# Kernel tuning notes

Measured on AMD Instinct MI355X. Metric: run time of the kernel, lower is better.

Reference implementation:

```python
import jax, jax.numpy as jnp
import numpy as np

N, E, R, H = 50000, 800000, 8, 1  # nodes, edges, relations, heads
IN_DIM = HID = OUT = 128
NEG_SLOPE = 0.2  # PyG RGATConv default


def _rgat_layer(x, W, q, k, b, src, dst, etype):
    """One RGATConv (additive-self-attention, across-relation softmax, dim=1).
    x: [N, Cin]; W: [R, Cin, H*C]; q,k: [H*C, H]; b: [H*C]."""
    n = x.shape[0]
    xr = jnp.einsum('nc,rcd->rnd', x, W)            # [R, N, H*C] per-relation transform
    qproj = jnp.einsum('rnd,dh->rnh', xr, q)        # [R, N, H]
    kproj = jnp.einsum('rnd,dh->rnh', xr, k)        # [R, N, H]
    out_j = xr[etype, src]                          # [E, H*C] transformed source feats
    alpha = jax.nn.leaky_relu(qproj[etype, dst] + kproj[etype, src], NEG_SLOPE)  # [E, H]
    # per-destination-node softmax over incoming edges (across relations)
    amax = jax.ops.segment_max(alpha, dst, num_segments=n)
    amax = jnp.where(jnp.isfinite(amax), amax, 0.0)
    ex = jnp.exp(alpha - amax[dst])                 # [E, H]
    denom = jax.ops.segment_sum(ex, dst, num_segments=n)
    alpha = ex / (denom[dst] + 1e-16)
    d = out_j.shape[1]
    c = d // H
    msg = (alpha[:, :, None] * out_j.reshape(-1, H, c)).reshape(-1, d)  # [E, H*C]
    out = jax.ops.segment_sum(msg, dst, num_segments=n)                  # [N, H*C]
    return out + b


def setup_inputs() -> dict:
    key = jax.random.key(0)
    ks = jax.random.split(key, 16)
    inp = {
        'x': jax.random.normal(ks[0], (N, IN_DIM), dtype=jnp.float32),
        'edge_index': jax.random.randint(ks[1], (2, E), 0, N, dtype=jnp.int32),
        'edge_type': jax.random.randint(ks[2], (E,), 0, R, dtype=jnp.int32),
    }
    dims = [(IN_DIM, HID), (HID, HID), (HID, OUT)]
    for i, (cin, cout) in enumerate(dims):
        d = H * cout
        s = 1.0 / np.sqrt(cin)
        inp[f'W{i}'] = jax.random.normal(ks[3 + 4 * i], (R, cin, d), dtype=jnp.float32) * s
        inp[f'q{i}'] = jax.random.normal(ks[4 + 4 * i], (d, H), dtype=jnp.float32) * (1.0 / np.sqrt(d))
        inp[f'k{i}'] = jax.random.normal(ks[5 + 4 * i], (d, H), dtype=jnp.float32) * (1.0 / np.sqrt(d))
        inp[f'b{i}'] = jnp.zeros((d,), dtype=jnp.float32)
    return inp


def reference(x, edge_index, edge_type, W0, q0, k0, b0, W1, q1, k1, b1, W2, q2, k2, b2):
    src, dst = edge_index[0], edge_index[1]
    h = jax.nn.relu(_rgat_layer(x, W0, q0, k0, b0, src, dst, edge_type))
    h = jax.nn.relu(_rgat_layer(h, W1, q1, k1, b1, src, dst, edge_type))
    return _rgat_layer(h, W2, q2, k2, b2, src, dst, edge_type)
```

## Files before the change

kernel.cpp:

```cpp
#include <hip/hip_runtime.h>
#include <hip/hip_bf16.h>
#include <cstdint>
#include <cstddef>

#define NNODES 50000
#define NEDGES 800000
#define NREL 8
#define DIM 128
#define NOUT 1024
#define NEG_SLOPE 0.2f

typedef __attribute__((ext_vector_type(8))) short short8;
typedef __attribute__((ext_vector_type(4))) float f32x4;

static __device__ __forceinline__ short f2bf(float v) {
  union { float f; unsigned u; } c; c.f = v;
  unsigned u = c.u;
  unsigned r = (u + 0x7fffu + ((u >> 16) & 1u)) >> 16;
  return (short)r;
}
static __device__ __forceinline__ float bf2f(short s) {
  union { unsigned u; float f; } c; c.u = ((unsigned)(unsigned short)s) << 16;
  return c.f;
}


__global__ void k_hist(const int* __restrict__ ei, const int* __restrict__ et,
                       int* __restrict__ cnt, int E) {
  int e = blockIdx.x * 256 + threadIdx.x;
  if (e < E) {
    int d = ei[E + e];
    int t = et[e];
    atomicAdd(&cnt[d * NREL + t], 1);
  }
}

__global__ void k_scan_reduce(const int* __restrict__ cnt, int* __restrict__ sums, int n) {
  __shared__ int sd[256];
  int base = blockIdx.x * 4096;
  int t = threadIdx.x;
  int acc = 0;
  for (int i = t; i < 4096; i += 256) {
    int idx = base + i;
    if (idx < n) acc += cnt[idx];
  }
  sd[t] = acc; __syncthreads();
  for (int s = 128; s > 0; s >>= 1) {
    if (t < s) sd[t] += sd[t + s];
    __syncthreads();
  }
  if (t == 0) sums[blockIdx.x] = sd[0];
}

__global__ void k_scan_top(int* sums, int nb) {
  if (threadIdx.x == 0 && blockIdx.x == 0) {
    int run = 0;
    for (int i = 0; i < nb; i++) { int v = sums[i]; sums[i] = run; run += v; }
  }
}

__global__ void k_scan_final(const int* __restrict__ cnt, const int* __restrict__ sums,
                             int* __restrict__ offs, int n, int E) {
  __shared__ int sd[256];
  int base = blockIdx.x * 4096;
  int t = threadIdx.x;
  int run = sums[blockIdx.x];
  for (int c = 0; c < 16; c++) {
    int idx = base + c * 256 + t;
    int v = (idx < n) ? cnt[idx] : 0;
    sd[t] = v; __syncthreads();
    for (int s = 1; s < 256; s <<= 1) {
      int u = (t >= s) ? sd[t - s] : 0;
      __syncthreads();
      sd[t] += u;
      __syncthreads();
    }
    if (idx < n) offs[idx] = run + sd[t] - v;
    run += sd[255];
    __syncthreads();
  }
  if (blockIdx.x == 0 && t == 0) offs[n] = E;
}

__global__ void k_scatter(const int* __restrict__ ei, const int* __restrict__ et,
                          int* __restrict__ cursor, int* __restrict__ pk, int E) {
  int e = blockIdx.x * 256 + threadIdx.x;
  if (e < E) {
    int s = ei[e];
    int d = ei[E + e];
    int t = et[e];
    int pos = atomicAdd(&cursor[d * NREL + t], 1);
    pk[pos] = s | (t << 16);
  }
}


__global__ void k_splitW_frag(const float* __restrict__ W, short* __restrict__ Wfh,
                              short* __restrict__ Wfl) {
  int id = blockIdx.x * 256 + threadIdx.x;
  if (id >= 16384) return;
  int l = id & 63;
  int kc = (id >> 6) & 3;
  int n16 = id >> 8;
  int n = n16 * 16 + (l & 15);
  int r = n >> 7, nn = n & 127;
  int k0 = kc * 32 + (l >> 4) * 8;
  short8 vh, vl;
#pragma unroll
  for (int j = 0; j < 8; j++) {
    float v = W[((size_t)r * DIM + k0 + j) * DIM + nn];
    short h = f2bf(v);
    vh[j] = h;
    vl[j] = f2bf(v - bf2f(h));
  }
  ((short8*)Wfh)[id] = vh;
  ((short8*)Wfl)[id] = vl;
}

__global__ void k_wqk(const float* __restrict__ W, const float* __restrict__ q,
                      const float* __restrict__ k, float* __restrict__ wq,
                      float* __restrict__ wk) {
  int id = blockIdx.x * 256 + threadIdx.x;
  if (id >= 2 * NREL * DIM) return;
  int which = id >> 10;
  int rc = id & 1023;
  const float* wrow = W + (size_t)rc * DIM;
  const float* v = which ? k : q;
  float acc = 0.f;
#pragma unroll 8
  for (int d = 0; d < DIM; d++) acc += wrow[d] * v[d];
  (which ? wk : wq)[rc] = acc;
}

__global__ void k_qk(const float* __restrict__ x, const float* __restrict__ wq,
                     const float* __restrict__ wk, float* __restrict__ qp,
                     float* __restrict__ kp, int N) {
  int wid = (blockIdx.x * blockDim.x + threadIdx.x) >> 6;
  int lane = threadIdx.x & 63;
  if (wid >= N) return;
  float x0 = x[(size_t)wid * DIM + lane];
  float x1 = x[(size_t)wid * DIM + 64 + lane];
#pragma unroll
  for (int r = 0; r < NREL; r++) {
    float aq = x0 * wq[r * DIM + lane] + x1 * wq[r * DIM + 64 + lane];
    float ak = x0 * wk[r * DIM + lane] + x1 * wk[r * DIM + 64 + lane];
    for (int s = 32; s > 0; s >>= 1) {
      aq += __shfl_xor(aq, s);
      ak += __shfl_xor(ak, s);
    }
    if (lane == 0) {
      qp[(size_t)wid * NREL + r] = aq;
      kp[(size_t)wid * NREL + r] = ak;
    }
  }
}

#define XR_SPITCH 132

__global__ __launch_bounds__(256, 3) void k_xr(
    const float* __restrict__ A, const short* __restrict__ Wfh,
    const short* __restrict__ Wfl, float* __restrict__ xr, int M) {
  __shared__ float sA[64 * XR_SPITCH];
  int t = threadIdx.x, w = t >> 6, l = t & 63;
  int m0 = blockIdx.x * 64;
  int nb = blockIdx.y;
  {
    int row = t >> 2, seg = t & 3;
    int m = m0 + row;
    const float* src = A + (size_t)m * DIM + seg * 32;
    float4 z = make_float4(0.f, 0.f, 0.f, 0.f);
#pragma unroll
    for (int q = 0; q < 8; q++) {
      float4 v = (m < M) ? *(const float4*)(src + q * 4) : z;
      *(float4*)(&sA[row * XR_SPITCH + seg * 32 + q * 4]) = v;
    }
  }
  __syncthreads();
  f32x4 acc[4][4];
  f32x4 zero = {0.f, 0.f, 0.f, 0.f};
#pragma unroll
  for (int mt = 0; mt < 4; mt++)
#pragma unroll
    for (int nt = 0; nt < 4; nt++) acc[mt][nt] = zero;

  int r16 = l & 15, hi16 = l >> 4;
  int n16base = nb * 16 + w * 4;
#pragma unroll
  for (int kc = 0; kc < 4; kc++) {
    short8 fsh[4], fsl[4];
#pragma unroll
    for (int mt = 0; mt < 4; mt++) {
      const float* ps = &sA[(mt * 16 + r16) * XR_SPITCH + kc * 32 + hi16 * 8];
      f32x4 va = *(const f32x4*)ps;
      f32x4 vb = *(const f32x4*)(ps + 4);
      short8 hh, ll;
#pragma unroll
      for (int jj = 0; jj < 4; jj++) {
        short h = f2bf(va[jj]);
        hh[jj] = h; ll[jj] = f2bf(va[jj] - bf2f(h));
      }
#pragma unroll
      for (int jj = 0; jj < 4; jj++) {
        short h = f2bf(vb[jj]);
        hh[4 + jj] = h; ll[4 + jj] = f2bf(vb[jj] - bf2f(h));
      }
      fsh[mt] = hh; fsl[mt] = ll;
    }
#pragma unroll
    for (int nt = 0; nt < 4; nt++) {
      size_t fid = ((size_t)(n16base + nt) * 4 + kc) * 64 + l;
      short8 ah = ((const short8*)Wfh)[fid];
      short8 al = ((const short8*)Wfl)[fid];
#pragma unroll
      for (int mt = 0; mt < 4; mt++) {
        acc[mt][nt] = __builtin_amdgcn_mfma_f32_16x16x32_bf16(ah, fsh[mt], acc[mt][nt], 0, 0, 0);
        acc[mt][nt] = __builtin_amdgcn_mfma_f32_16x16x32_bf16(ah, fsl[mt], acc[mt][nt], 0, 0, 0);
        acc[mt][nt] = __builtin_amdgcn_mfma_f32_16x16x32_bf16(al, fsh[mt], acc[mt][nt], 0, 0, 0);
      }
    }
  }
#pragma unroll
  for (int mt = 0; mt < 4; mt++) {
    int m = m0 + mt * 16 + r16;
    if (m >= M) continue;
#pragma unroll
    for (int nt = 0; nt < 4; nt++) {
      int n = nb * 256 + w * 64 + nt * 16 + hi16 * 4;
      f32x4 a = acc[mt][nt];
      float4 o; o.x = a.x; o.y = a.y; o.z = a.z; o.w = a.w;
      *(float4*)(xr + (size_t)m * NOUT + n) = o;
    }
  }
}

__global__ void k_agg_out(const float* __restrict__ xr, const float* __restrict__ qp,
                          const float* __restrict__ kp, const int* __restrict__ offs,
                          const int* __restrict__ pk, const float* __restrict__ bias,
                          float* __restrict__ out, int N, int relu) {
  int wid = (blockIdx.x * blockDim.x + threadIdx.x) >> 6;
  int lane = threadIdx.x & 63;
  if (wid >= N) return;
  int base = wid * NREL;
  int start = offs[base], end = offs[base + NREL];
  float a0 = 0.f, a1 = 0.f;
  if (start < end) {
    float m = -1e30f;
    for (int i = start + lane; i < end; i += 64) {
      int p = pk[i];
      int src = p & 0xffff, tt = p >> 16;
      float a = qp[base + tt] + kp[src * NREL + tt];
      a = (a > 0.f) ? a : NEG_SLOPE * a;
      m = fmaxf(m, a);
    }
    for (int s = 32; s > 0; s >>= 1) m = fmaxf(m, __shfl_xor(m, s));
    float ssum = 0.f;
    for (int i = start + lane; i < end; i += 64) {
      int p = pk[i];
      int src = p & 0xffff, tt = p >> 16;
      float a = qp[base + tt] + kp[src * NREL + tt];
      a = (a > 0.f) ? a : NEG_SLOPE * a;
      ssum += expf(a - m);
    }
    for (int s = 32; s > 0; s >>= 1) ssum += __shfl_xor(ssum, s);
    float inv = 1.f / (ssum + 1e-16f);
    for (int i = start; i < end; i += 2) {
      int p0 = pk[i];
      int has1 = (i + 1 < end);
      int p1 = pk[has1 ? i + 1 : i];
      int s0 = p0 & 0xffff, t0 = p0 >> 16;
      int s1 = p1 & 0xffff, t1 = p1 >> 16;
      float2 xv0 = ((const float2*)(xr + ((size_t)s0 * NREL + t0) * DIM))[lane];
      float2 xv1 = ((const float2*)(xr + ((size_t)s1 * NREL + t1) * DIM))[lane];
      float e0a = qp[base + t0] + kp[s0 * NREL + t0];
      e0a = (e0a > 0.f) ? e0a : NEG_SLOPE * e0a;
      float w0 = expf(e0a - m) * inv;
      float e1a = qp[base + t1] + kp[s1 * NREL + t1];
      e1a = (e1a > 0.f) ? e1a : NEG_SLOPE * e1a;
      float w1 = has1 ? (expf(e1a - m) * inv) : 0.f;
      a0 = fmaf(w0, xv0.x, a0);
      a1 = fmaf(w0, xv0.y, a1);
      a0 = fmaf(w1, xv1.x, a0);
      a1 = fmaf(w1, xv1.y, a1);
    }
  }
  float2 bv = ((const float2*)bias)[lane];
  a0 += bv.x; a1 += bv.y;
  if (relu) { a0 = fmaxf(a0, 0.f); a1 = fmaxf(a1, 0.f); }
  float2 o; o.x = a0; o.y = a1;
  ((float2*)(out + (size_t)wid * DIM))[lane] = o;
}


extern "C" void kernel_launch(void* const* d_in, const int* in_sizes, int n_in,
                              void* d_out, int out_size, void* d_ws, size_t ws_size,
                              hipStream_t stream) {
  const float* x = (const float*)d_in[0];
  const int* ei = (const int*)d_in[1];
  const int* et = (const int*)d_in[2];
  const float* Wl3[3] = {(const float*)d_in[3], (const float*)d_in[7], (const float*)d_in[11]};
  const float* ql[3] = {(const float*)d_in[4], (const float*)d_in[8], (const float*)d_in[12]};
  const float* kl[3] = {(const float*)d_in[5], (const float*)d_in[9], (const float*)d_in[13]};
  const float* bl[3] = {(const float*)d_in[6], (const float*)d_in[10], (const float*)d_in[14]};
  float* out = (float*)d_out;

  char* w = (char*)d_ws;
  auto alloc = [&](size_t bytes) -> char* {
    char* p = w;
    w += (bytes + 255) & ~(size_t)255;
    return p;
  };
  const int NK = NNODES * NREL;
  float* xr = (float*)alloc((size_t)NNODES * NOUT * 4);
  int* cnt = (int*)alloc((size_t)NK * 4);
  int* offs = (int*)alloc((size_t)(NK + 1) * 4);
  int* cursor = (int*)alloc((size_t)NK * 4);
  int* sums = (int*)alloc(256 * 4);
  int* pk = (int*)alloc((size_t)NEDGES * 4);
  float* wq = (float*)alloc((size_t)NREL * DIM * 4);
  float* wk = (float*)alloc((size_t)NREL * DIM * 4);
  float* qp = (float*)alloc((size_t)NNODES * NREL * 4);
  float* kp = (float*)alloc((size_t)NNODES * NREL * 4);
  short* Wfh = (short*)alloc((size_t)DIM * NOUT * 2);
  short* Wfl = (short*)alloc((size_t)DIM * NOUT * 2);
  float* h1 = (float*)alloc((size_t)NNODES * DIM * 4);
  float* h2 = (float*)alloc((size_t)NNODES * DIM * 4);

  hipMemsetAsync(cnt, 0, (size_t)NK * 4, stream);
  k_hist<<<(NEDGES + 255) / 256, 256, 0, stream>>>(ei, et, cnt, NEDGES);
  int nchunk = (NK + 4095) / 4096;
  k_scan_reduce<<<nchunk, 256, 0, stream>>>(cnt, sums, NK);
  k_scan_top<<<1, 64, 0, stream>>>(sums, nchunk);
  k_scan_final<<<nchunk, 256, 0, stream>>>(cnt, sums, offs, NK, NEDGES);
  hipMemcpyAsync(cursor, offs, (size_t)NK * 4, hipMemcpyDeviceToDevice, stream);
  k_scatter<<<(NEDGES + 255) / 256, 256, 0, stream>>>(ei, et, cursor, pk, NEDGES);

  const float* hin = x;
  float* houts[3] = {h1, h2, out};
  for (int l = 0; l < 3; l++) {
    k_splitW_frag<<<64, 256, 0, stream>>>(Wl3[l], Wfh, Wfl);
    k_wqk<<<(2 * NREL * DIM + 255) / 256, 256, 0, stream>>>(Wl3[l], ql[l], kl[l], wq, wk);
    k_qk<<<(NNODES + 3) / 4, 256, 0, stream>>>(hin, wq, wk, qp, kp, NNODES);
    dim3 gxr((NNODES + 63) / 64, 4);
    k_xr<<<gxr, 256, 0, stream>>>(hin, Wfh, Wfl, xr, NNODES);
    k_agg_out<<<(NNODES + 3) / 4, 256, 0, stream>>>(xr, qp, kp, offs, pk, bl[l],
                                                    houts[l], NNODES, l < 2 ? 1 : 0);
    hin = houts[l];
  }
}
```

Baseline: 946.1 us.

## Rework xr GEMM tiling, use online softmax in aggregation, fuse prep kernels

Several unrelated changes land together. The xr GEMM now splits A into bf16 hi/lo parts once, in a swizzled shared-memory layout, instead of splitting inside the inner loop per wave. It also halves the N-tile per block, remaps blocks so neighbouring tiles share an XCD, and raises occupancy via launch bounds. The aggregation kernel merges the max and sum passes into one online-softmax pass, uses fast __expf, and unrolls the gather loop by 4. On the setup side, the top-level scan is parallelised, the cursor copy is folded into scan_final, and the weight-split and wq/wk kernels are merged into one launch, trading a little precision in the exponentials for fewer passes and launches.

```diff
diff --git a/kernel.cpp b/kernel.cpp
--- a/kernel.cpp
+++ b/kernel.cpp
@@ -53,14 +53,22 @@
 }
 
 __global__ void k_scan_top(int* sums, int nb) {
-  if (threadIdx.x == 0 && blockIdx.x == 0) {
-    int run = 0;
-    for (int i = 0; i < nb; i++) { int v = sums[i]; sums[i] = run; run += v; }
-  }
+  __shared__ int sd[128];
+  int t = threadIdx.x;
+  int v = (t < nb) ? sums[t] : 0;
+  sd[t] = v; __syncthreads();
+  for (int s = 1; s < 128; s <<= 1) {
+    int u = (t >= s) ? sd[t - s] : 0;
+    __syncthreads();
+    sd[t] += u;
+    __syncthreads();
+  }
+  if (t < nb) sums[t] = sd[t] - v;
 }
 
 __global__ void k_scan_final(const int* __restrict__ cnt, const int* __restrict__ sums,
-                             int* __restrict__ offs, int n, int E) {
+                             int* __restrict__ offs, int* __restrict__ cur,
+                             int n, int E) {
   __shared__ int sd[256];
   int base = blockIdx.x * 4096;
   int t = threadIdx.x;
@@ -75,7 +83,11 @@
       sd[t] += u;
       __syncthreads();
     }
-    if (idx < n) offs[idx] = run + sd[t] - v;
+    if (idx < n) {
+      int e0 = run + sd[t] - v;
+      offs[idx] = e0;
+      cur[idx] = e0;
+    }
     run += sd[255];
     __syncthreads();
   }
@@ -95,41 +107,40 @@
 }
 
 
-__global__ void k_splitW_frag(const float* __restrict__ W, short* __restrict__ Wfh,
-                              short* __restrict__ Wfl) {
-  int id = blockIdx.x * 256 + threadIdx.x;
-  if (id >= 16384) return;
-  int l = id & 63;
-  int kc = (id >> 6) & 3;
-  int n16 = id >> 8;
-  int n = n16 * 16 + (l & 15);
-  int r = n >> 7, nn = n & 127;
-  int k0 = kc * 32 + (l >> 4) * 8;
-  short8 vh, vl;
-#pragma unroll
-  for (int j = 0; j < 8; j++) {
-    float v = W[((size_t)r * DIM + k0 + j) * DIM + nn];
-    short h = f2bf(v);
-    vh[j] = h;
-    vl[j] = f2bf(v - bf2f(h));
-  }
-  ((short8*)Wfh)[id] = vh;
-  ((short8*)Wfl)[id] = vl;
-}
-
-__global__ void k_wqk(const float* __restrict__ W, const float* __restrict__ q,
-                      const float* __restrict__ k, float* __restrict__ wq,
-                      float* __restrict__ wk) {
-  int id = blockIdx.x * 256 + threadIdx.x;
-  if (id >= 2 * NREL * DIM) return;
-  int which = id >> 10;
-  int rc = id & 1023;
-  const float* wrow = W + (size_t)rc * DIM;
-  const float* v = which ? k : q;
-  float acc = 0.f;
+__global__ void k_wprep(const float* __restrict__ W, const float* __restrict__ q,
+                        const float* __restrict__ k, short* __restrict__ Wfh,
+                        short* __restrict__ Wfl, float* __restrict__ wq,
+                        float* __restrict__ wk) {
+  int b = blockIdx.x;
+  if (b < 64) {
+    int id = b * 256 + threadIdx.x;
+    int l = id & 63;
+    int kc = (id >> 6) & 3;
+    int n16 = id >> 8;
+    int n = n16 * 16 + (l & 15);
+    int r = n >> 7, nn = n & 127;
+    int k0 = kc * 32 + (l >> 4) * 8;
+    short8 vh, vl;
+#pragma unroll
+    for (int j = 0; j < 8; j++) {
+      float v = W[((size_t)r * DIM + k0 + j) * DIM + nn];
+      short h = f2bf(v);
+      vh[j] = h;
+      vl[j] = f2bf(v - bf2f(h));
+    }
+    ((short8*)Wfh)[id] = vh;
+    ((short8*)Wfl)[id] = vl;
+  } else {
+    int id = (b - 64) * 256 + threadIdx.x;
+    int which = id >> 10;
+    int rc = id & 1023;
+    const float* wrow = W + (size_t)rc * DIM;
+    const float* v = which ? k : q;
+    float acc = 0.f;
 #pragma unroll 8
-  for (int d = 0; d < DIM; d++) acc += wrow[d] * v[d];
-  (which ? wk : wq)[rc] = acc;
+    for (int d = 0; d < DIM; d++) acc += wrow[d] * v[d];
+    (which ? wk : wq)[rc] = acc;
+  }
 }
 
 __global__ void k_qk(const float* __restrict__ x, const float* __restrict__ wq,
@@ -155,59 +166,64 @@
   }
 }
 
-#define XR_SPITCH 132
-
-__global__ __launch_bounds__(256, 3) void k_xr(
+__global__ __launch_bounds__(256, 4) void k_xr(
     const float* __restrict__ A, const short* __restrict__ Wfh,
-    const short* __restrict__ Wfl, float* __restrict__ xr, int M) {
-  __shared__ float sA[64 * XR_SPITCH];
+    const short* __restrict__ Wfl, float* __restrict__ xr, int M, int nmt) {
+  __shared__ char sAh[64 * 256];
+  __shared__ char sAl[64 * 256];
+  int lin = blockIdx.x;
+  int xcd = lin & 7, pos = lin >> 3;
+  int g = xcd * nmt + pos;
+  int mt0 = g >> 3, nb = g & 7;
+  int m0 = mt0 * 64;
   int t = threadIdx.x, w = t >> 6, l = t & 63;
-  int m0 = blockIdx.x * 64;
-  int nb = blockIdx.y;
+
   {
-    int row = t >> 2, seg = t & 3;
+    int row = t >> 2, q4 = t & 3;
     int m = m0 + row;
-    const float* src = A + (size_t)m * DIM + seg * 32;
+    int sw = (row & 7) << 4;
+    const float4* src = (const float4*)(A + (size_t)m * DIM + q4 * 32);
     float4 z = make_float4(0.f, 0.f, 0.f, 0.f);
 #pragma unroll
-    for (int q = 0; q < 8; q++) {
-      float4 v = (m < M) ? *(const float4*)(src + q * 4) : z;
-      *(float4*)(&sA[row * XR_SPITCH + seg * 32 + q * 4]) = v;
+    for (int u = 0; u < 4; u++) {
+      float4 va = (m < M) ? src[2 * u] : z;
+      float4 vb = (m < M) ? src[2 * u + 1] : z;
+      float vv[8] = {va.x, va.y, va.z, va.w, vb.x, vb.y, vb.z, vb.w};
+      short8 hh, ll;
+#pragma unroll
+      for (int j = 0; j < 8; j++) {
+        short h = f2bf(vv[j]);
+        hh[j] = h;
+        ll[j] = f2bf(vv[j] - bf2f(h));
+      }
+      int off = row * 256 + ((q4 * 64 + u * 16) ^ sw);
+      *(short8*)(sAh + off) = hh;
+      *(short8*)(sAl + off) = ll;
     }
   }
   __syncthreads();
-  f32x4 acc[4][4];
+
+  f32x4 acc[4][2];
   f32x4 zero = {0.f, 0.f, 0.f, 0.f};
 #pragma unroll
   for (int mt = 0; mt < 4; mt++)
 #pragma unroll
-    for (int nt = 0; nt < 4; nt++) acc[mt][nt] = zero;
+    for (int nt = 0; nt < 2; nt++) acc[mt][nt] = zero;
 
   int r16 = l & 15, hi16 = l >> 4;
-  int n16base = nb * 16 + w * 4;
+  int n16base = nb * 8 + w * 2;
 #pragma unroll
   for (int kc = 0; kc < 4; kc++) {
     short8 fsh[4], fsl[4];
 #pragma unroll
     for (int mt = 0; mt < 4; mt++) {
-      const float* ps = &sA[(mt * 16 + r16) * XR_SPITCH + kc * 32 + hi16 * 8];
-      f32x4 va = *(const f32x4*)ps;
-      f32x4 vb = *(const f32x4*)(ps + 4);
-      short8 hh, ll;
-#pragma unroll
-      for (int jj = 0; jj < 4; jj++) {
-        short h = f2bf(va[jj]);
-        hh[jj] = h; ll[jj] = f2bf(va[jj] - bf2f(h));
-      }
-#pragma unroll
-      for (int jj = 0; jj < 4; jj++) {
-        short h = f2bf(vb[jj]);
-        hh[4 + jj] = h; ll[4 + jj] = f2bf(vb[jj] - bf2f(h));
-      }
-      fsh[mt] = hh; fsl[mt] = ll;
-    }
-#pragma unroll
-    for (int nt = 0; nt < 4; nt++) {
+      int row = mt * 16 + r16;
+      int off = row * 256 + ((kc * 64 + hi16 * 16) ^ ((row & 7) << 4));
+      fsh[mt] = *(const short8*)(sAh + off);
+      fsl[mt] = *(const short8*)(sAl + off);
+    }
+#pragma unroll
+    for (int nt = 0; nt < 2; nt++) {
       size_t fid = ((size_t)(n16base + nt) * 4 + kc) * 64 + l;
       short8 ah = ((const short8*)Wfh)[fid];
       short8 al = ((const short8*)Wfl)[fid];
@@ -224,8 +240,8 @@
     int m = m0 + mt * 16 + r16;
     if (m >= M) continue;
 #pragma unroll
-    for (int nt = 0; nt < 4; nt++) {
-      int n = nb * 256 + w * 64 + nt * 16 + hi16 * 4;
+    for (int nt = 0; nt < 2; nt++) {
+      int n = nb * 128 + w * 32 + nt * 16 + hi16 * 4;
       f32x4 a = acc[mt][nt];
       float4 o; o.x = a.x; o.y = a.y; o.z = a.z; o.w = a.w;
       *(float4*)(xr + (size_t)m * NOUT + n) = o;
@@ -244,43 +260,57 @@
   int start = offs[base], end = offs[base + NREL];
   float a0 = 0.f, a1 = 0.f;
   if (start < end) {
-    float m = -1e30f;
+    float m = -1e30f, s = 0.f;
     for (int i = start + lane; i < end; i += 64) {
       int p = pk[i];
       int src = p & 0xffff, tt = p >> 16;
       float a = qp[base + tt] + kp[src * NREL + tt];
       a = (a > 0.f) ? a : NEG_SLOPE * a;
-      m = fmaxf(m, a);
-    }
-    for (int s = 32; s > 0; s >>= 1) m = fmaxf(m, __shfl_xor(m, s));
-    float ssum = 0.f;
-    for (int i = start + lane; i < end; i += 64) {
+      float mn = fmaxf(m, a);
+      s = s * __expf(m - mn) + __expf(a - mn);
+      m = mn;
+    }
+    for (int d = 32; d > 0; d >>= 1) {
+      float mo = __shfl_xor(m, d);
+      float so = __shfl_xor(s, d);
+      float mn = fmaxf(m, mo);
+      s = s * __expf(m - mn) + so * __expf(mo - mn);
+      m = mn;
+    }
+    float inv = 1.f / (s + 1e-16f);
+    int i = start;
+    for (; i + 4 <= end; i += 4) {
+      int p0 = pk[i], p1 = pk[i + 1], p2 = pk[i + 2], p3 = pk[i + 3];
+      float2 xv0 = ((const float2*)(xr + (((size_t)(p0 & 0xffff)) * NREL + (p0 >> 16)) * DIM))[lane];
+      float2 xv1 = ((const float2*)(xr + (((size_t)(p1 & 0xffff)) * NREL + (p1 >> 16)) * DIM))[lane];
+      float2 xv2 = ((const float2*)(xr + (((size_t)(p2 & 0xffff)) * NREL + (p2 >> 16)) * DIM))[lane];
+      float2 xv3 = ((const float2*)(xr + (((size_t)(p3 & 0xffff)) * NREL + (p3 >> 16)) * DIM))[lane];
+      float aa0 = qp[base + (p0 >> 16)] + kp[(p0 & 0xffff) * NREL + (p0 >> 16)];
+      float aa1 = qp[base + (p1 >> 16)] + kp[(p1 & 0xffff) * NREL + (p1 >> 16)];
+      float aa2 = qp[base + (p2 >> 16)] + kp[(p2 & 0xffff) * NREL + (p2 >> 16)];
+      float aa3 = qp[base + (p3 >> 16)] + kp[(p3 & 0xffff) * NREL + (p3 >> 16)];
+      aa0 = (aa0 > 0.f) ? aa0 : NEG_SLOPE * aa0;
+      aa1 = (aa1 > 0.f) ? aa1 : NEG_SLOPE * aa1;
+      aa2 = (aa2 > 0.f) ? aa2 : NEG_SLOPE * aa2;
+      aa3 = (aa3 > 0.f) ? aa3 : NEG_SLOPE * aa3;
+      float w0 = __expf(aa0 - m) * inv;
+      float w1 = __expf(aa1 - m) * inv;
+      float w2 = __expf(aa2 - m) * inv;
+      float w3 = __expf(aa3 - m) * inv;
+      a0 = fmaf(w0, xv0.x, a0); a1 = fmaf(w0, xv0.y, a1);
+      a0 = fmaf(w1, xv1.x, a0); a1 = fmaf(w1, xv1.y, a1);
+      a0 = fmaf(w2, xv2.x, a0); a1 = fmaf(w2, xv2.y, a1);
+      a0 = fmaf(w3, xv3.x, a0); a1 = fmaf(w3, xv3.y, a1);
+    }
+    for (; i < end; i++) {
       int p = pk[i];
       int src = p & 0xffff, tt = p >> 16;
+      float2 xv = ((const float2*)(xr + ((size_t)src * NREL + tt) * DIM))[lane];
       float a = qp[base + tt] + kp[src * NREL + tt];
       a = (a > 0.f) ? a : NEG_SLOPE * a;
-      ssum += expf(a - m);
-    }
-    for (int s = 32; s > 0; s >>= 1) ssum += __shfl_xor(ssum, s);
-    float inv = 1.f / (ssum + 1e-16f);
-    for (int i = start; i < end; i += 2) {
-      int p0 = pk[i];
-      int has1 = (i + 1 < end);
-      int p1 = pk[has1 ? i + 1 : i];
-      int s0 = p0 & 0xffff, t0 = p0 >> 16;
-      int s1 = p1 & 0xffff, t1 = p1 >> 16;
-      float2 xv0 = ((const float2*)(xr + ((size_t)s0 * NREL + t0) * DIM))[lane];
-      float2 xv1 = ((const float2*)(xr + ((size_t)s1 * NREL + t1) * DIM))[lane];
-      float e0a = qp[base + t0] + kp[s0 * NREL + t0];
-      e0a = (e0a > 0.f) ? e0a : NEG_SLOPE * e0a;
-      float w0 = expf(e0a - m) * inv;
-      float e1a = qp[base + t1] + kp[s1 * NREL + t1];
-      e1a = (e1a > 0.f) ? e1a : NEG_SLOPE * e1a;
-      float w1 = has1 ? (expf(e1a - m) * inv) : 0.f;
-      a0 = fmaf(w0, xv0.x, a0);
-      a1 = fmaf(w0, xv0.y, a1);
-      a0 = fmaf(w1, xv1.x, a0);
-      a1 = fmaf(w1, xv1.y, a1);
+      float wg = __expf(a - m) * inv;
+      a0 = fmaf(wg, xv.x, a0);
+      a1 = fmaf(wg, xv.y, a1);
     }
   }
   float2 bv = ((const float2*)bias)[lane];
@@ -329,19 +359,17 @@
   k_hist<<<(NEDGES + 255) / 256, 256, 0, stream>>>(ei, et, cnt, NEDGES);
   int nchunk = (NK + 4095) / 4096;
   k_scan_reduce<<<nchunk, 256, 0, stream>>>(cnt, sums, NK);
-  k_scan_top<<<1, 64, 0, stream>>>(sums, nchunk);
-  k_scan_final<<<nchunk, 256, 0, stream>>>(cnt, sums, offs, NK, NEDGES);
-  hipMemcpyAsync(cursor, offs, (size_t)NK * 4, hipMemcpyDeviceToDevice, stream);
+  k_scan_top<<<1, 128, 0, stream>>>(sums, nchunk);
+  k_scan_final<<<nchunk, 256, 0, stream>>>(cnt, sums, offs, cursor, NK, NEDGES);
   k_scatter<<<(NEDGES + 255) / 256, 256, 0, stream>>>(ei, et, cursor, pk, NEDGES);
 
   const float* hin = x;
   float* houts[3] = {h1, h2, out};
+  const int nmt = (NNODES + 63) / 64;
   for (int l = 0; l < 3; l++) {
-    k_splitW_frag<<<64, 256, 0, stream>>>(Wl3[l], Wfh, Wfl);
-    k_wqk<<<(2 * NREL * DIM + 255) / 256, 256, 0, stream>>>(Wl3[l], ql[l], kl[l], wq, wk);
+    k_wprep<<<72, 256, 0, stream>>>(Wl3[l], ql[l], kl[l], Wfh, Wfl, wq, wk);
     k_qk<<<(NNODES + 3) / 4, 256, 0, stream>>>(hin, wq, wk, qp, kp, NNODES);
-    dim3 gxr((NNODES + 63) / 64, 4);
-    k_xr<<<gxr, 256, 0, stream>>>(hin, Wfh, Wfl, xr, NNODES);
+    k_xr<<<nmt * 8, 256, 0, stream>>>(hin, Wfh, Wfl, xr, NNODES, nmt);
     k_agg_out<<<(NNODES + 3) / 4, 256, 0, stream>>>(xr, qp, kp, offs, pk, bl[l],
                                                     houts[l], NNODES, l < 2 ? 1 : 0);
     hin = houts[l];
```

Measured after the change: 1.070 ms. 1.13x slower.
